# Optimization experiments

Measured on AMD Instinct MI355X. Metric: run time of the kernel, lower is better.

Reference implementation:

```python
import jax, jax.numpy as jnp
import numpy as np
import math

B, C, H, W = 2, 64, 64, 64
DI = 2 * C          # d_inner
N = 16              # d_state
R = math.ceil(C / 16)  # dt_rank
K = 3               # d_conv
L = H * W

PARAM_KEYS = [
    'pe_x_w', 'pe_x_b', 'rms_x_w', 'conv_x_w', 'conv_x_b',
    'pe_info_w', 'pe_info_b', 'rms_info_w', 'conv_info_w', 'conv_info_b',
    'pe_mask_w', 'pe_mask_b', 'rms_mask_w', 'conv_mask_w', 'conv_mask_b',
    'in_x_w', 'in_info_w', 'in_mask_w',
    'delta_w', 'dt_w', 'dt_b', 'B_w', 'C_w', 'A_log', 'out_w',
]


def setup_inputs():
    key = jax.random.key(0)
    ki = iter(jax.random.split(key, 40))
    def nrm(shape, scale=1.0):
        return jax.random.normal(next(ki), shape, jnp.float32) * scale
    sc, sdi, sr, sk = 1/np.sqrt(C), 1/np.sqrt(DI), 1/np.sqrt(R), 1/np.sqrt(K)
    inp = {}
    for name in ('up', 'mask', 'x', 'y', 'z'):
        inp[name] = nrm((B, C, H, W))
    for role in ('x', 'info', 'mask'):
        inp[f'pe_{role}_w'] = nrm((3, C, C), sc)
        inp[f'pe_{role}_b'] = jnp.zeros((3, C), jnp.float32)
        inp[f'rms_{role}_w'] = jnp.ones((3, C), jnp.float32)
        inp[f'conv_{role}_w'] = nrm((3, DI, K), sk)
        inp[f'conv_{role}_b'] = nrm((3, DI), sk)
    inp['in_x_w'] = nrm((3, 2 * DI, C), sc)
    inp['in_info_w'] = nrm((3, DI, C), sc)
    inp['in_mask_w'] = nrm((3, DI, C), sc)
    inp['delta_w'] = nrm((3, R, DI), sdi)
    inp['dt_w'] = nrm((3, DI, R), sr)
    rng = np.random.default_rng(0)
    dt = np.exp(rng.uniform(size=(3, DI)) * (np.log(0.1) - np.log(0.001)) + np.log(0.001)).clip(min=1e-4)
    inp['dt_b'] = jnp.asarray(np.log(-np.expm1(-dt)), jnp.float32)
    inp['B_w'] = nrm((3, N, DI), sdi)
    inp['C_w'] = nrm((3, N, DI), sdi)
    inp['A_log'] = jnp.tile(jnp.log(jnp.arange(1, N + 1, dtype=jnp.float32)), (3, DI, 1))
    inp['out_w'] = nrm((3, C, DI), sdi)
    return inp


def embed1x1(t, w, b):
    # PatchEmbed with patch_size=1: 1x1 conv then flatten to [B, L, C]
    y = jnp.einsum('bchw,oc->bohw', t, w) + b[None, :, None, None]
    bb, cc, hh, ww = y.shape
    return y.reshape(bb, cc, hh * ww).transpose(0, 2, 1)


def rms_norm(x, w, eps=1e-5):
    return x * jax.lax.rsqrt(jnp.mean(x * x, axis=-1, keepdims=True) + eps) * w


def causal_dwconv_silu(x, w, b):
    # x [B, D, L]; depthwise causal conv1d (left-pad K-1), then SiLU
    kk = w.shape[1]
    xp = jnp.pad(x, ((0, 0), (0, 0), (kk - 1, 0)))
    y = jax.lax.conv_general_dilated(
        xp, w[:, None, :], window_strides=(1,), padding='VALID',
        dimension_numbers=('NCH', 'OIH', 'NCH'), feature_group_count=w.shape[0])
    return jax.nn.silu(y + b[None, :, None])


def selective_scan(u, delta, A, Bm, Cm):
    # u, delta: [B, D, L]; A: [D, N]; Bm, Cm: [B, N, L]
    dA = jnp.exp(jnp.einsum('bdl,dn->lbdn', delta, A))           # [L,B,D,N]
    dBu = jnp.einsum('bdl,bnl,bdl->lbdn', delta, Bm, u)          # [L,B,D,N]
    Ct = Cm.transpose(2, 0, 1)                                   # [L,B,N]
    h0 = jnp.zeros((u.shape[0], u.shape[1], A.shape[1]), u.dtype)
    def step(h, inp):
        dA_t, dBu_t, C_t = inp
        h = dA_t * h + dBu_t
        return h, jnp.einsum('bdn,bn->bd', h, C_t)
    _, ys = jax.lax.scan(step, h0, (dA, dBu, Ct))
    return ys.transpose(1, 2, 0)                                 # [B,D,L]


def branch(xin, maskin, upin, p):
    bb, cc, hh, ww = xin.shape
    xe = rms_norm(embed1x1(xin, p['pe_x_w'], p['pe_x_b']), p['rms_x_w'])        # [B,L,C]
    xz = jnp.einsum('blc,dc->bdl', xe, p['in_x_w'])                              # [B,2DI,L]
    di = xz.shape[1] // 2
    xc, x_act = xz[:, :di], xz[:, di:]
    info = rms_norm(embed1x1(upin, p['pe_info_w'], p['pe_info_b']), p['rms_info_w'])
    info = jnp.einsum('blc,dc->bdl', info, p['in_info_w'])
    mk = rms_norm(embed1x1(maskin, p['pe_mask_w'], p['pe_mask_b']), p['rms_mask_w'])
    mk = jnp.einsum('blc,dc->bdl', mk, p['in_mask_w'])
    xc = causal_dwconv_silu(xc, p['conv_x_w'], p['conv_x_b'])
    mk = causal_dwconv_silu(mk, p['conv_mask_w'], p['conv_mask_b'])
    info = causal_dwconv_silu(info, p['conv_info_w'], p['conv_info_b'])
    # S6: delta from mask, B from info, C from x
    delta = jnp.einsum('bdl,rd->brl', mk, p['delta_w'])
    delta = jnp.einsum('brl,dr->bdl', delta, p['dt_w'])
    delta = jax.nn.softplus(delta + p['dt_b'][None, :, None])
    A = -jnp.exp(p['A_log'])
    Bm = jnp.einsum('bdl,nd->bnl', info, p['B_w'])
    Cm = jnp.einsum('bdl,nd->bnl', xc, p['C_w'])
    y = selective_scan(xc, delta, A, Bm, Cm)
    y = y * jax.nn.silu(x_act)
    y = jnp.einsum('bdl,cd->blc', y, p['out_w'])
    return y.transpose(0, 2, 1).reshape(bb, cc, hh, ww) + xin


def forward(up, mask, x, y, z, *params):
    pall = dict(zip(PARAM_KEYS, params))
    out = None
    for i, feat in enumerate((x, y, z)):
        p = {k: v[i] for k, v in pall.items()}
        o = branch(feat, mask, up, p)
        out = o if out is None else out + o
    return out


def reference(up, mask, x, y, z,
              pe_x_w, pe_x_b, rms_x_w, conv_x_w, conv_x_b,
              pe_info_w, pe_info_b, rms_info_w, conv_info_w, conv_info_b,
              pe_mask_w, pe_mask_b, rms_mask_w, conv_mask_w, conv_mask_b,
              in_x_w, in_info_w, in_mask_w,
              delta_w, dt_w, dt_b, B_w, C_w, A_log, out_w):
    return forward(up, mask, x, y, z,
                   pe_x_w, pe_x_b, rms_x_w, conv_x_w, conv_x_b,
                   pe_info_w, pe_info_b, rms_info_w, conv_info_w, conv_info_b,
                   pe_mask_w, pe_mask_b, rms_mask_w, conv_mask_w, conv_mask_b,
                   in_x_w, in_info_w, in_mask_w,
                   delta_w, dt_w, dt_b, B_w, C_w, A_log, out_w)
```

## Files before the change

kernel.cpp:

```cpp
#include <hip/hip_runtime.h>
#include <math.h>

namespace {

constexpr int NB = 3;
constexpr int BB = 2;
constexpr int CC = 64;
constexpr int LLEN = 4096;
constexpr int DI = 128;
constexpr int NN = 16;
constexpr int RR = 4;
constexpr int GG = 256;
constexpr int LC = 16;
constexpr int NSEQ = NB * BB * DI * NN;
constexpr size_t SBUF = (size_t)NB * BB * DI * LLEN;

typedef __attribute__((ext_vector_type(4))) float f32x4;
typedef __attribute__((ext_vector_type(8))) short bf16x8;

__device__ __forceinline__ float siluf(float v) { return v / (1.f + __expf(-v)); }

__device__ __forceinline__ short cvt_bf16(float f) {
    union { float f; unsigned u; } v; v.f = f;
    unsigned r = v.u + 0x7fffu + ((v.u >> 16) & 1u);
    return (short)(r >> 16);
}
__device__ __forceinline__ unsigned pack_bf16(float lo, float hi) {
    return ((unsigned)(unsigned short)cvt_bf16(hi) << 16) | (unsigned short)cvt_bf16(lo);
}
__device__ __forceinline__ bf16x8 pack8(float4 a, float4 b) {
    bf16x8 r;
    r[0] = cvt_bf16(a.x); r[1] = cvt_bf16(a.y); r[2] = cvt_bf16(a.z); r[3] = cvt_bf16(a.w);
    r[4] = cvt_bf16(b.x); r[5] = cvt_bf16(b.y); r[6] = cvt_bf16(b.z); r[7] = cvt_bf16(b.w);
    return r;
}

__global__ __launch_bounds__(256) void k1_embed(
    const float* __restrict__ up, const float* __restrict__ mask_,
    const float* __restrict__ fx, const float* __restrict__ fy, const float* __restrict__ fz,
    const float* __restrict__ pe_x_w, const float* __restrict__ pe_x_b, const float* __restrict__ rms_x_w,
    const float* __restrict__ pe_i_w, const float* __restrict__ pe_i_b, const float* __restrict__ rms_i_w,
    const float* __restrict__ pe_m_w, const float* __restrict__ pe_m_b, const float* __restrict__ rms_m_w,
    const float* __restrict__ in_x_w, const float* __restrict__ in_i_w, const float* __restrict__ in_m_w,
    float* __restrict__ xc_pre, float* __restrict__ x_act,
    float* __restrict__ info_pre, float* __restrict__ mk_pre)
{
    __shared__ short sE[64 * 64];
    __shared__ float red[4][64];
    __shared__ float sscl[64];

    int lt = blockIdx.x, job = blockIdx.y, b = blockIdx.z;
    int i = job / 3, r = job % 3;
    const float *src, *pw, *pb, *rw, *iw;
    if (r == 0) {
        src = (i == 0 ? fx : (i == 1 ? fy : fz));
        pw = pe_x_w + i * 4096; pb = pe_x_b + i * 64; rw = rms_x_w + i * 64;
        iw = in_x_w + (size_t)i * 256 * 64;
    } else if (r == 1) {
        src = up;
        pw = pe_i_w + i * 4096; pb = pe_i_b + i * 64; rw = rms_i_w + i * 64;
        iw = in_i_w + (size_t)i * 128 * 64;
    } else {
        src = mask_;
        pw = pe_m_w + i * 4096; pb = pe_m_b + i * 64; rw = rms_m_w + i * 64;
        iw = in_m_w + (size_t)i * 128 * 64;
    }
    int t = threadIdx.x;
    int w = t >> 6, lane = t & 63, lo = lane & 15, hi = lane >> 4;
    int l0 = lt * 64;
    const float* Xg = src + (size_t)b * 64 * LLEN;

    f32x4 acc1[4];
    #pragma unroll
    for (int nt = 0; nt < 4; ++nt) acc1[nt] = (f32x4){0.f, 0.f, 0.f, 0.f};

    #pragma unroll
    for (int ks = 0; ks < 2; ++ks) {
        const float* ap = pw + (16 * w + lo) * 64 + ks * 32 + hi * 8;
        bf16x8 a1 = pack8(*(const float4*)ap, *(const float4*)(ap + 4));
        #pragma unroll
        for (int nt = 0; nt < 4; ++nt) {
            const float* xc = Xg + (size_t)(ks * 32 + hi * 8) * LLEN + l0 + nt * 16 + lo;
            bf16x8 b1;
            #pragma unroll
            for (int j = 0; j < 8; ++j) b1[j] = cvt_bf16(xc[(size_t)j * LLEN]);
            acc1[nt] = __builtin_amdgcn_mfma_f32_16x16x32_bf16(a1, b1, acc1[nt], 0, 0, 0);
        }
    }

    float4 pbv = *(const float4*)&pb[16 * w + 4 * hi];
    float e_[4][4];
    #pragma unroll
    for (int nt = 0; nt < 4; ++nt) {
        e_[nt][0] = acc1[nt][0] + pbv.x;
        e_[nt][1] = acc1[nt][1] + pbv.y;
        e_[nt][2] = acc1[nt][2] + pbv.z;
        e_[nt][3] = acc1[nt][3] + pbv.w;
        float s = e_[nt][0] * e_[nt][0] + e_[nt][1] * e_[nt][1]
                + e_[nt][2] * e_[nt][2] + e_[nt][3] * e_[nt][3];
        s += __shfl_xor(s, 16);
        s += __shfl_xor(s, 32);
        if (lane < 16) red[w][nt * 16 + lo] = s;
    }
    __syncthreads();
    if (t < 64) {
        float s = red[0][t] + red[1][t] + red[2][t] + red[3][t];
        sscl[t] = rsqrtf(s * (1.f / 64.f) + 1e-5f);
    }
    __syncthreads();

    {
        int ob = 2 * w + (hi >> 1);
        #pragma unroll
        for (int nt = 0; nt < 4; ++nt) {
            float sc = sscl[16 * nt + lo];
            unsigned p0 = pack_bf16(e_[nt][0] * sc, e_[nt][1] * sc);
            unsigned p1 = pack_bf16(e_[nt][2] * sc, e_[nt][3] * sc);
            unsigned* p = (unsigned*)&sE[(16 * nt + lo) * 64 + (ob ^ (lo & 7)) * 8 + 4 * (hi & 1)];
            p[0] = p0; p[1] = p1;
        }
    }
    __syncthreads();

    bf16x8 b2[4][2];
    #pragma unroll
    for (int nt = 0; nt < 4; ++nt)
        #pragma unroll
        for (int ks = 0; ks < 2; ++ks) {
            int db = ks * 4 + hi;
            b2[nt][ks] = *(const bf16x8*)&sE[(16 * nt + lo) * 64 + (db ^ (lo & 7)) * 8];
        }

    size_t obase = ((size_t)(i * 2 + b)) * DI * LLEN;
    int MT = (r == 0) ? 4 : 2;
    for (int mm = 0; mm < MT; ++mm) {
        int m = MT * w + mm;
        bf16x8 a2[2];
        #pragma unroll
        for (int ks = 0; ks < 2; ++ks) {
            const float* wp = iw + (size_t)(16 * m + lo) * 64 + ks * 32 + hi * 8;
            float4 w0 = *(const float4*)wp;
            float4 w1 = *(const float4*)(wp + 4);
            float4 r0 = *(const float4*)&rw[ks * 32 + hi * 8];
            float4 r1 = *(const float4*)&rw[ks * 32 + hi * 8 + 4];
            w0.x *= r0.x; w0.y *= r0.y; w0.z *= r0.z; w0.w *= r0.w;
            w1.x *= r1.x; w1.y *= r1.y; w1.z *= r1.z; w1.w *= r1.w;
            a2[ks] = pack8(w0, w1);
        }
        f32x4 acc2[4];
        #pragma unroll
        for (int nt = 0; nt < 4; ++nt) acc2[nt] = (f32x4){0.f, 0.f, 0.f, 0.f};
        #pragma unroll
        for (int ks = 0; ks < 2; ++ks)
            #pragma unroll
            for (int nt = 0; nt < 4; ++nt)
                acc2[nt] = __builtin_amdgcn_mfma_f32_16x16x32_bf16(a2[ks], b2[nt][ks], acc2[nt], 0, 0, 0);

        int d0 = 16 * m + 4 * hi;
        float* dst; int dd = d0;
        if (r == 0) { if (d0 < 128) dst = xc_pre; else { dst = x_act; dd = d0 - 128; } }
        else if (r == 1) dst = info_pre;
        else dst = mk_pre;
        #pragma unroll
        for (int nt = 0; nt < 4; ++nt) {
            int l = l0 + 16 * nt + lo;
            *(float4*)&dst[obase + (size_t)l * DI + dd] =
                make_float4(acc2[nt][0], acc2[nt][1], acc2[nt][2], acc2[nt][3]);
        }
    }
}

__global__ __launch_bounds__(256) void k3_conv(
    const float* __restrict__ xc_pre, const float* __restrict__ info_pre, const float* __restrict__ mk_pre,
    const float* __restrict__ conv_x_w, const float* __restrict__ conv_x_b,
    const float* __restrict__ conv_i_w, const float* __restrict__ conv_i_b,
    const float* __restrict__ conv_m_w, const float* __restrict__ conv_m_b,
    const float* __restrict__ delta_w, const float* __restrict__ dt_w, const float* __restrict__ dt_b,
    const float* __restrict__ B_w, const float* __restrict__ C_w,
    float* __restrict__ u, float* __restrict__ delta,
    float* __restrict__ Bm, float* __restrict__ Cm)
{
    __shared__ __align__(16) float ot[64 * 128];
    __shared__ float rvec[4 * 64];

    int lt = blockIdx.x, ib = blockIdx.y, strm = blockIdx.z;
    int i = ib >> 1;
    int t = threadIdx.x;
    int l0 = lt * 64;
    size_t base = (size_t)ib * DI * LLEN;

    const float *inb, *cw, *cb;
    if (strm == 0)      { inb = mk_pre;   cw = conv_m_w + i * DI * 3; cb = conv_m_b + i * DI; }
    else if (strm == 1) { inb = info_pre; cw = conv_i_w + i * DI * 3; cb = conv_i_b + i * DI; }
    else                { inb = xc_pre;   cw = conv_x_w + i * DI * 3; cb = conv_x_b + i * DI; }

    {
        int d4 = t & 31, lq = t >> 5;
        int d = d4 * 4;
        float cw0[4], cw1[4], cw2[4], cbb[4];
        #pragma unroll
        for (int j = 0; j < 4; ++j) {
            cw0[j] = cw[(d + j) * 3 + 0];
            cw1[j] = cw[(d + j) * 3 + 1];
            cw2[j] = cw[(d + j) * 3 + 2];
            cbb[j] = cb[d + j];
        }
        int gl0 = l0 + lq * 8;
        float4 x0 = make_float4(0.f, 0.f, 0.f, 0.f), x1 = x0;
        if (gl0 >= 2) x0 = *(const float4*)&inb[base + (size_t)(gl0 - 2) * DI + d];
        if (gl0 >= 1) x1 = *(const float4*)&inb[base + (size_t)(gl0 - 1) * DI + d];
        #pragma unroll
        for (int li = 0; li < 8; ++li) {
            int l = lq * 8 + li;
            float4 x2 = *(const float4*)&inb[base + (size_t)(gl0 + li) * DI + d];
            float4 v;
            v.x = siluf(cw0[0] * x0.x + cw1[0] * x1.x + cw2[0] * x2.x + cbb[0]);
            v.y = siluf(cw0[1] * x0.y + cw1[1] * x1.y + cw2[1] * x2.y + cbb[1]);
            v.z = siluf(cw0[2] * x0.z + cw1[2] * x1.z + cw2[2] * x2.z + cbb[2]);
            v.w = siluf(cw0[3] * x0.w + cw1[3] * x1.w + cw2[3] * x2.w + cbb[3]);
            *(float4*)&ot[l * 128 + ((d4 * 4) ^ ((l & 7) << 2))] = v;
            if (strm == 2) *(float4*)&u[base + (size_t)(gl0 + li) * DI + d] = v;
            x0 = x1; x1 = x2;
        }
    }
    __syncthreads();

    if (strm == 0) {
        {
            int l = t & 63, r = t >> 6, sw = (l & 7) << 2;
            const float* dw = delta_w + i * RR * DI + r * DI;
            float acc = 0.f;
            #pragma unroll
            for (int d4 = 0; d4 < 32; ++d4) {
                float4 v = *(const float4*)&ot[l * 128 + ((d4 * 4) ^ sw)];
                int db = d4 * 4;
                acc += dw[db] * v.x + dw[db + 1] * v.y + dw[db + 2] * v.z + dw[db + 3] * v.w;
            }
            rvec[r * 64 + l] = acc;
        }
        __syncthreads();
        {
            int d = t & 127, lh = t >> 7;
            const float* dtw = dt_w + i * DI * RR + d * RR;
            float w0 = dtw[0], w1 = dtw[1], w2 = dtw[2], w3 = dtw[3];
            float bb = dt_b[i * DI + d];
            #pragma unroll 4
            for (int li = 0; li < 32; ++li) {
                int l = lh * 32 + li;
                float v = bb + w0 * rvec[l] + w1 * rvec[64 + l] + w2 * rvec[128 + l] + w3 * rvec[192 + l];
                float sp = (v > 20.f) ? v : log1pf(__expf(v));
                delta[base + (size_t)(l0 + l) * DI + d] = sp;
            }
        }
    } else {
        int l = t & 63, ng = t >> 6, sw = (l & 7) << 2;
        const float* wv = ((strm == 1) ? B_w : C_w) + i * NN * DI + ng * 4 * DI;
        float a0 = 0.f, a1 = 0.f, a2 = 0.f, a3 = 0.f;
        #pragma unroll
        for (int d4 = 0; d4 < 32; ++d4) {
            float4 v = *(const float4*)&ot[l * 128 + ((d4 * 4) ^ sw)];
            int db = d4 * 4;
            a0 += wv[db] * v.x + wv[db + 1] * v.y + wv[db + 2] * v.z + wv[db + 3] * v.w;
            a1 += wv[DI + db] * v.x + wv[DI + db + 1] * v.y + wv[DI + db + 2] * v.z + wv[DI + db + 3] * v.w;
            a2 += wv[2 * DI + db] * v.x + wv[2 * DI + db + 1] * v.y + wv[2 * DI + db + 2] * v.z + wv[2 * DI + db + 3] * v.w;
            a3 += wv[3 * DI + db] * v.x + wv[3 * DI + db + 1] * v.y + wv[3 * DI + db + 2] * v.z + wv[3 * DI + db + 3] * v.w;
        }
        float* dst = (strm == 1) ? Bm : Cm;
        *(float4*)&dst[((size_t)ib * LLEN + l0 + l) * NN + ng * 4] = make_float4(a0, a1, a2, a3);
    }
}

__global__ __launch_bounds__(128) void k4_scan1(
    const float* __restrict__ u, const float* __restrict__ delta,
    const float* __restrict__ Bm, const float* __restrict__ A_log,
    float* __restrict__ aprod, float* __restrict__ hend)
{
    __shared__ __align__(16) float sB[LC * 16];
    int g = blockIdx.x, ib = blockIdx.y, i = ib >> 1;
    int d = threadIdx.x;
    if (d < LC * 16 / 4)
        ((float4*)sB)[d] = ((const float4*)(Bm + ((size_t)ib * LLEN + (size_t)g * LC) * NN))[d];
    float A[16], h[16];
    {
        const float4* al = (const float4*)(A_log + ((size_t)i * DI + d) * NN);
        #pragma unroll
        for (int q = 0; q < 4; ++q) {
            float4 v = al[q];
            A[4 * q] = -__expf(v.x); A[4 * q + 1] = -__expf(v.y);
            A[4 * q + 2] = -__expf(v.z); A[4 * q + 3] = -__expf(v.w);
        }
    }
    #pragma unroll
    for (int n = 0; n < 16; ++n) h[n] = 0.f;
    float sdl = 0.f;
    __syncthreads();
    size_t base = ((size_t)ib * LLEN + (size_t)g * LC) * DI + d;
    #pragma unroll 4
    for (int li = 0; li < LC; ++li) {
        float dl = delta[base + li * DI];
        float du = dl * u[base + li * DI];
        sdl += dl;
        const float4* bl = (const float4*)(sB + li * 16);
        float4 b0 = bl[0], b1 = bl[1], b2 = bl[2], b3 = bl[3];
        h[0] = __expf(dl * A[0]) * h[0] + du * b0.x;  h[1] = __expf(dl * A[1]) * h[1] + du * b0.y;
        h[2] = __expf(dl * A[2]) * h[2] + du * b0.z;  h[3] = __expf(dl * A[3]) * h[3] + du * b0.w;
        h[4] = __expf(dl * A[4]) * h[4] + du * b1.x;  h[5] = __expf(dl * A[5]) * h[5] + du * b1.y;
        h[6] = __expf(dl * A[6]) * h[6] + du * b1.z;  h[7] = __expf(dl * A[7]) * h[7] + du * b1.w;
        h[8] = __expf(dl * A[8]) * h[8] + du * b2.x;  h[9] = __expf(dl * A[9]) * h[9] + du * b2.y;
        h[10] = __expf(dl * A[10]) * h[10] + du * b2.z; h[11] = __expf(dl * A[11]) * h[11] + du * b2.w;
        h[12] = __expf(dl * A[12]) * h[12] + du * b3.x; h[13] = __expf(dl * A[13]) * h[13] + du * b3.y;
        h[14] = __expf(dl * A[14]) * h[14] + du * b3.z; h[15] = __expf(dl * A[15]) * h[15] + du * b3.w;
    }
    size_t seq = ((size_t)ib * DI + d) * NN;
    float4* ap = (float4*)(aprod + (size_t)g * NSEQ + seq);
    float4* he = (float4*)(hend + (size_t)g * NSEQ + seq);
    #pragma unroll
    for (int q = 0; q < 4; ++q) {
        ap[q] = make_float4(__expf(A[4 * q] * sdl), __expf(A[4 * q + 1] * sdl),
                            __expf(A[4 * q + 2] * sdl), __expf(A[4 * q + 3] * sdl));
        he[q] = make_float4(h[4 * q], h[4 * q + 1], h[4 * q + 2], h[4 * q + 3]);
    }
}

__global__ __launch_bounds__(256) void k5_prefix(
    const float* __restrict__ aprod, const float* __restrict__ hend,
    float* __restrict__ hin)
{
    int s = blockIdx.x * 256 + threadIdx.x;
    float h = 0.f;
    #pragma unroll 8
    for (int g = 0; g < GG; ++g) {
        hin[(size_t)g * NSEQ + s] = h;
        h = aprod[(size_t)g * NSEQ + s] * h + hend[(size_t)g * NSEQ + s];
    }
}

__global__ __launch_bounds__(128) void k6_scan2(
    const float* __restrict__ u, const float* __restrict__ delta,
    const float* __restrict__ Bm, const float* __restrict__ Cm,
    const float* __restrict__ A_log, const float* __restrict__ hin,
    float* __restrict__ y)
{
    __shared__ __align__(16) float sB[LC * 16];
    __shared__ __align__(16) float sC[LC * 16];
    int g = blockIdx.x, ib = blockIdx.y, i = ib >> 1;
    int d = threadIdx.x;
    {
        const float4* bsrc = (const float4*)(Bm + ((size_t)ib * LLEN + (size_t)g * LC) * NN);
        const float4* csrc = (const float4*)(Cm + ((size_t)ib * LLEN + (size_t)g * LC) * NN);
        if (d < 64) ((float4*)sB)[d] = bsrc[d];
        else ((float4*)sC)[d - 64] = csrc[d - 64];
    }
    float A[16], h[16];
    {
        const float4* al = (const float4*)(A_log + ((size_t)i * DI + d) * NN);
        #pragma unroll
        for (int q = 0; q < 4; ++q) {
            float4 v = al[q];
            A[4 * q] = -__expf(v.x); A[4 * q + 1] = -__expf(v.y);
            A[4 * q + 2] = -__expf(v.z); A[4 * q + 3] = -__expf(v.w);
        }
    }
    {
        size_t seq = ((size_t)ib * DI + d) * NN;
        const float4* hp = (const float4*)(hin + (size_t)g * NSEQ + seq);
        #pragma unroll
        for (int q = 0; q < 4; ++q) {
            float4 v = hp[q];
            h[4 * q] = v.x; h[4 * q + 1] = v.y; h[4 * q + 2] = v.z; h[4 * q + 3] = v.w;
        }
    }
    __syncthreads();
    size_t base = ((size_t)ib * LLEN + (size_t)g * LC) * DI + d;
    #pragma unroll 4
    for (int li = 0; li < LC; ++li) {
        float dl = delta[base + li * DI];
        float du = dl * u[base + li * DI];
        const float4* bl = (const float4*)(sB + li * 16);
        const float4* cl = (const float4*)(sC + li * 16);
        float4 b0 = bl[0], b1 = bl[1], b2 = bl[2], b3 = bl[3];
        float4 c0 = cl[0], c1 = cl[1], c2 = cl[2], c3 = cl[3];
        float acc = 0.f;
        h[0] = __expf(dl * A[0]) * h[0] + du * b0.x;  acc += h[0] * c0.x;
        h[1] = __expf(dl * A[1]) * h[1] + du * b0.y;  acc += h[1] * c0.y;
        h[2] = __expf(dl * A[2]) * h[2] + du * b0.z;  acc += h[2] * c0.z;
        h[3] = __expf(dl * A[3]) * h[3] + du * b0.w;  acc += h[3] * c0.w;
        h[4] = __expf(dl * A[4]) * h[4] + du * b1.x;  acc += h[4] * c1.x;
        h[5] = __expf(dl * A[5]) * h[5] + du * b1.y;  acc += h[5] * c1.y;
        h[6] = __expf(dl * A[6]) * h[6] + du * b1.z;  acc += h[6] * c1.z;
        h[7] = __expf(dl * A[7]) * h[7] + du * b1.w;  acc += h[7] * c1.w;
        h[8] = __expf(dl * A[8]) * h[8] + du * b2.x;  acc += h[8] * c2.x;
        h[9] = __expf(dl * A[9]) * h[9] + du * b2.y;  acc += h[9] * c2.y;
        h[10] = __expf(dl * A[10]) * h[10] + du * b2.z; acc += h[10] * c2.z;
        h[11] = __expf(dl * A[11]) * h[11] + du * b2.w; acc += h[11] * c2.w;
        h[12] = __expf(dl * A[12]) * h[12] + du * b3.x; acc += h[12] * c3.x;
        h[13] = __expf(dl * A[13]) * h[13] + du * b3.y; acc += h[13] * c3.y;
        h[14] = __expf(dl * A[14]) * h[14] + du * b3.z; acc += h[14] * c3.z;
        h[15] = __expf(dl * A[15]) * h[15] + du * b3.w; acc += h[15] * c3.w;
        y[base + li * DI] = acc;
    }
}

__global__ __launch_bounds__(256) void k7_out(
    const float* __restrict__ y, const float* __restrict__ xact,
    const float* __restrict__ out_w,
    const float* __restrict__ fx, const float* __restrict__ fy, const float* __restrict__ fz,
    float* __restrict__ out)
{
    __shared__ short sG[64 * 128];
    int lt = blockIdx.x, b = blockIdx.y;
    int l0 = lt * 64;
    int t = threadIdx.x;
    int w = t >> 6, lane = t & 63, lo = lane & 15, hi = lane >> 4;

    f32x4 acc[4];
    #pragma unroll
    for (int nt = 0; nt < 4; ++nt) acc[nt] = (f32x4){0.f, 0.f, 0.f, 0.f};

    for (int i = 0; i < 3; ++i) {
        size_t base = ((size_t)(i * 2 + b)) * DI * LLEN;
        __syncthreads();
        #pragma unroll
        for (int p = 0; p < 8; ++p) {
            int idx = t + 256 * p;
            int d4 = idx & 31, l = idx >> 5;
            int d = d4 * 4;
            float4 yv = *(const float4*)&y[base + (size_t)(l0 + l) * DI + d];
            float4 xa = *(const float4*)&xact[base + (size_t)(l0 + l) * DI + d];
            float g0 = yv.x * siluf(xa.x), g1 = yv.y * siluf(xa.y);
            float g2 = yv.z * siluf(xa.z), g3 = yv.w * siluf(xa.w);
            int blk = d4 >> 1;
            int blks = (blk & 8) | ((blk ^ (l & 7)) & 7);
            unsigned* p32 = (unsigned*)&sG[l * 128 + blks * 8 + 4 * (d4 & 1)];
            p32[0] = pack_bf16(g0, g1);
            p32[1] = pack_bf16(g2, g3);
        }
        __syncthreads();

        const float* ow = out_w + (size_t)i * CC * DI;
        bf16x8 a[4];
        #pragma unroll
        for (int ks = 0; ks < 4; ++ks) {
            const float* ap = ow + (size_t)(16 * w + lo) * 128 + ks * 32 + hi * 8;
            a[ks] = pack8(*(const float4*)ap, *(const float4*)(ap + 4));
        }
        #pragma unroll
        for (int nt = 0; nt < 4; ++nt) {
            int l = 16 * nt + lo;
            #pragma unroll
            for (int ks = 0; ks < 4; ++ks) {
                int db = ks * 4 + hi;
                int blks = (db & 8) | ((db ^ (l & 7)) & 7);
                bf16x8 bv = *(const bf16x8*)&sG[l * 128 + blks * 8];
                acc[nt] = __builtin_amdgcn_mfma_f32_16x16x32_bf16(a[ks], bv, acc[nt], 0, 0, 0);
            }
        }
    }

    #pragma unroll
    for (int nt = 0; nt < 4; ++nt) {
        int l = l0 + 16 * nt + lo;
        int cbase = 16 * w + 4 * hi;
        #pragma unroll
        for (int rr = 0; rr < 4; ++rr) {
            int c = cbase + rr;
            size_t idx = ((size_t)b * CC + c) * LLEN + l;
            out[idx] = acc[nt][rr] + fx[idx] + fy[idx] + fz[idx];
        }
    }
}

}

extern "C" void kernel_launch(void* const* d_in, const int* in_sizes, int n_in,
                              void* d_out, int out_size, void* d_ws, size_t ws_size,
                              hipStream_t stream)
{
    (void)in_sizes; (void)n_in; (void)out_size; (void)ws_size;
    const float* up       = (const float*)d_in[0];
    const float* mask_    = (const float*)d_in[1];
    const float* fx       = (const float*)d_in[2];
    const float* fy       = (const float*)d_in[3];
    const float* fz       = (const float*)d_in[4];
    const float* pe_x_w   = (const float*)d_in[5];
    const float* pe_x_b   = (const float*)d_in[6];
    const float* rms_x_w  = (const float*)d_in[7];
    const float* conv_x_w = (const float*)d_in[8];
    const float* conv_x_b = (const float*)d_in[9];
    const float* pe_i_w   = (const float*)d_in[10];
    const float* pe_i_b   = (const float*)d_in[11];
    const float* rms_i_w  = (const float*)d_in[12];
    const float* conv_i_w = (const float*)d_in[13];
    const float* conv_i_b = (const float*)d_in[14];
    const float* pe_m_w   = (const float*)d_in[15];
    const float* pe_m_b   = (const float*)d_in[16];
    const float* rms_m_w  = (const float*)d_in[17];
    const float* conv_m_w = (const float*)d_in[18];
    const float* conv_m_b = (const float*)d_in[19];
    const float* in_x_w   = (const float*)d_in[20];
    const float* in_i_w   = (const float*)d_in[21];
    const float* in_m_w   = (const float*)d_in[22];
    const float* delta_w  = (const float*)d_in[23];
    const float* dt_w     = (const float*)d_in[24];
    const float* dt_b     = (const float*)d_in[25];
    const float* B_w      = (const float*)d_in[26];
    const float* C_w      = (const float*)d_in[27];
    const float* A_log    = (const float*)d_in[28];
    const float* out_w    = (const float*)d_in[29];
    float* out = (float*)d_out;

    float* ws = (float*)d_ws;
    const size_t S = SBUF;
    float* xc_pre   = ws;
    float* x_act    = ws + S;
    float* info_pre = ws + 2 * S;
    float* mk_pre   = ws + 3 * S;
    float* ubuf     = ws + 4 * S;
    float* dbuf     = ws + 5 * S;
    float* BmB      = ws + 6 * S;
    float* CmB      = BmB + (size_t)NB * BB * NN * LLEN;
    float* aprod = info_pre;
    float* hendb = mk_pre;
    float* hinb  = xc_pre;
    float* ybuf  = info_pre;

    hipLaunchKernelGGL(k1_embed, dim3(64, 9, 2), dim3(256), 0, stream,
        up, mask_, fx, fy, fz,
        pe_x_w, pe_x_b, rms_x_w, pe_i_w, pe_i_b, rms_i_w, pe_m_w, pe_m_b, rms_m_w,
        in_x_w, in_i_w, in_m_w, xc_pre, x_act, info_pre, mk_pre);

    hipLaunchKernelGGL(k3_conv, dim3(64, 6, 3), dim3(256), 0, stream,
        xc_pre, info_pre, mk_pre,
        conv_x_w, conv_x_b, conv_i_w, conv_i_b, conv_m_w, conv_m_b,
        delta_w, dt_w, dt_b, B_w, C_w, ubuf, dbuf, BmB, CmB);

    hipLaunchKernelGGL(k4_scan1, dim3(GG, 6), dim3(128), 0, stream,
        ubuf, dbuf, BmB, A_log, aprod, hendb);

    hipLaunchKernelGGL(k5_prefix, dim3(NSEQ / 256), dim3(256), 0, stream,
        aprod, hendb, hinb);

    hipLaunchKernelGGL(k6_scan2, dim3(GG, 6), dim3(128), 0, stream,
        ubuf, dbuf, BmB, CmB, A_log, hinb, ybuf);

    hipLaunchKernelGGL(k7_out, dim3(64, 2), dim3(256), 0, stream,
        ybuf, x_act, out_w, fx, fy, fz, out);
}
```

Measured before the change: 134.6 us.

## Store all intermediate workspace buffers in fp16 instead of fp32

Every intermediate buffer passed between kernels changes from fp32 to fp16: the projected activations, u, delta, B/C, the chunk products and end states, the carried-in states and y. Math inside each kernel stays fp32, with conversion on load and store. This halves global memory traffic across the memory-bound pipeline of embed, conv, two-pass scan and output. The cost is precision: fp16 range and rounding on delta, state products and hidden states can add error across the chunked scan.

```diff
diff --git a/kernel.cpp b/kernel.cpp
--- a/kernel.cpp
+++ b/kernel.cpp
@@ -15,8 +15,11 @@
 constexpr int NSEQ = NB * BB * DI * NN;
 constexpr size_t SBUF = (size_t)NB * BB * DI * LLEN;
 
+typedef _Float16 f16;
 typedef __attribute__((ext_vector_type(4))) float f32x4;
 typedef __attribute__((ext_vector_type(8))) short bf16x8;
+typedef __attribute__((ext_vector_type(4))) _Float16 f16x4;
+typedef __attribute__((ext_vector_type(8))) _Float16 f16x8;
 
 __device__ __forceinline__ float siluf(float v) { return v / (1.f + __expf(-v)); }
 
@@ -33,6 +36,12 @@
     r[0] = cvt_bf16(a.x); r[1] = cvt_bf16(a.y); r[2] = cvt_bf16(a.z); r[3] = cvt_bf16(a.w);
     r[4] = cvt_bf16(b.x); r[5] = cvt_bf16(b.y); r[6] = cvt_bf16(b.z); r[7] = cvt_bf16(b.w);
     return r;
+}
+__device__ __forceinline__ f16x4 to_h4(float a, float b, float c, float d) {
+    f16x4 r; r[0] = (f16)a; r[1] = (f16)b; r[2] = (f16)c; r[3] = (f16)d; return r;
+}
+__device__ __forceinline__ float4 to_f4(f16x4 v) {
+    return make_float4((float)v[0], (float)v[1], (float)v[2], (float)v[3]);
 }
 
 __global__ __launch_bounds__(256) void k1_embed(
@@ -42,8 +51,8 @@
     const float* __restrict__ pe_i_w, const float* __restrict__ pe_i_b, const float* __restrict__ rms_i_w,
     const float* __restrict__ pe_m_w, const float* __restrict__ pe_m_b, const float* __restrict__ rms_m_w,
     const float* __restrict__ in_x_w, const float* __restrict__ in_i_w, const float* __restrict__ in_m_w,
-    float* __restrict__ xc_pre, float* __restrict__ x_act,
-    float* __restrict__ info_pre, float* __restrict__ mk_pre)
+    f16* __restrict__ xc_pre, f16* __restrict__ x_act,
+    f16* __restrict__ info_pre, f16* __restrict__ mk_pre)
 {
     __shared__ short sE[64 * 64];
     __shared__ float red[4][64];
@@ -157,28 +166,28 @@
                 acc2[nt] = __builtin_amdgcn_mfma_f32_16x16x32_bf16(a2[ks], b2[nt][ks], acc2[nt], 0, 0, 0);
 
         int d0 = 16 * m + 4 * hi;
-        float* dst; int dd = d0;
+        f16* dst; int dd = d0;
         if (r == 0) { if (d0 < 128) dst = xc_pre; else { dst = x_act; dd = d0 - 128; } }
         else if (r == 1) dst = info_pre;
         else dst = mk_pre;
         #pragma unroll
         for (int nt = 0; nt < 4; ++nt) {
             int l = l0 + 16 * nt + lo;
-            *(float4*)&dst[obase + (size_t)l * DI + dd] =
-                make_float4(acc2[nt][0], acc2[nt][1], acc2[nt][2], acc2[nt][3]);
+            *(f16x4*)&dst[obase + (size_t)l * DI + dd] =
+                to_h4(acc2[nt][0], acc2[nt][1], acc2[nt][2], acc2[nt][3]);
         }
     }
 }
 
 __global__ __launch_bounds__(256) void k3_conv(
-    const float* __restrict__ xc_pre, const float* __restrict__ info_pre, const float* __restrict__ mk_pre,
+    const f16* __restrict__ xc_pre, const f16* __restrict__ info_pre, const f16* __restrict__ mk_pre,
     const float* __restrict__ conv_x_w, const float* __restrict__ conv_x_b,
     const float* __restrict__ conv_i_w, const float* __restrict__ conv_i_b,
     const float* __restrict__ conv_m_w, const float* __restrict__ conv_m_b,
     const float* __restrict__ delta_w, const float* __restrict__ dt_w, const float* __restrict__ dt_b,
     const float* __restrict__ B_w, const float* __restrict__ C_w,
-    float* __restrict__ u, float* __restrict__ delta,
-    float* __restrict__ Bm, float* __restrict__ Cm)
+    f16* __restrict__ u, f16* __restrict__ delta,
+    f16* __restrict__ Bm, f16* __restrict__ Cm)
 {
     __shared__ __align__(16) float ot[64 * 128];
     __shared__ float rvec[4 * 64];
@@ -189,7 +198,7 @@
     int l0 = lt * 64;
     size_t base = (size_t)ib * DI * LLEN;
 
-    const float *inb, *cw, *cb;
+    const f16 *inb; const float *cw, *cb;
     if (strm == 0)      { inb = mk_pre;   cw = conv_m_w + i * DI * 3; cb = conv_m_b + i * DI; }
     else if (strm == 1) { inb = info_pre; cw = conv_i_w + i * DI * 3; cb = conv_i_b + i * DI; }
     else                { inb = xc_pre;   cw = conv_x_w + i * DI * 3; cb = conv_x_b + i * DI; }
@@ -207,19 +216,19 @@
         }
         int gl0 = l0 + lq * 8;
         float4 x0 = make_float4(0.f, 0.f, 0.f, 0.f), x1 = x0;
-        if (gl0 >= 2) x0 = *(const float4*)&inb[base + (size_t)(gl0 - 2) * DI + d];
-        if (gl0 >= 1) x1 = *(const float4*)&inb[base + (size_t)(gl0 - 1) * DI + d];
+        if (gl0 >= 2) x0 = to_f4(*(const f16x4*)&inb[base + (size_t)(gl0 - 2) * DI + d]);
+        if (gl0 >= 1) x1 = to_f4(*(const f16x4*)&inb[base + (size_t)(gl0 - 1) * DI + d]);
         #pragma unroll
         for (int li = 0; li < 8; ++li) {
             int l = lq * 8 + li;
-            float4 x2 = *(const float4*)&inb[base + (size_t)(gl0 + li) * DI + d];
+            float4 x2 = to_f4(*(const f16x4*)&inb[base + (size_t)(gl0 + li) * DI + d]);
             float4 v;
             v.x = siluf(cw0[0] * x0.x + cw1[0] * x1.x + cw2[0] * x2.x + cbb[0]);
             v.y = siluf(cw0[1] * x0.y + cw1[1] * x1.y + cw2[1] * x2.y + cbb[1]);
             v.z = siluf(cw0[2] * x0.z + cw1[2] * x1.z + cw2[2] * x2.z + cbb[2]);
             v.w = siluf(cw0[3] * x0.w + cw1[3] * x1.w + cw2[3] * x2.w + cbb[3]);
             *(float4*)&ot[l * 128 + ((d4 * 4) ^ ((l & 7) << 2))] = v;
-            if (strm == 2) *(float4*)&u[base + (size_t)(gl0 + li) * DI + d] = v;
+            if (strm == 2) *(f16x4*)&u[base + (size_t)(gl0 + li) * DI + d] = to_h4(v.x, v.y, v.z, v.w);
             x0 = x1; x1 = x2;
         }
     }
@@ -249,7 +258,7 @@
                 int l = lh * 32 + li;
                 float v = bb + w0 * rvec[l] + w1 * rvec[64 + l] + w2 * rvec[128 + l] + w3 * rvec[192 + l];
                 float sp = (v > 20.f) ? v : log1pf(__expf(v));
-                delta[base + (size_t)(l0 + l) * DI + d] = sp;
+                delta[base + (size_t)(l0 + l) * DI + d] = (f16)sp;
             }
         }
     } else {
@@ -265,21 +274,23 @@
             a2 += wv[2 * DI + db] * v.x + wv[2 * DI + db + 1] * v.y + wv[2 * DI + db + 2] * v.z + wv[2 * DI + db + 3] * v.w;
             a3 += wv[3 * DI + db] * v.x + wv[3 * DI + db + 1] * v.y + wv[3 * DI + db + 2] * v.z + wv[3 * DI + db + 3] * v.w;
         }
-        float* dst = (strm == 1) ? Bm : Cm;
-        *(float4*)&dst[((size_t)ib * LLEN + l0 + l) * NN + ng * 4] = make_float4(a0, a1, a2, a3);
+        f16* dst = (strm == 1) ? Bm : Cm;
+        *(f16x4*)&dst[((size_t)ib * LLEN + l0 + l) * NN + ng * 4] = to_h4(a0, a1, a2, a3);
     }
 }
 
 __global__ __launch_bounds__(128) void k4_scan1(
-    const float* __restrict__ u, const float* __restrict__ delta,
-    const float* __restrict__ Bm, const float* __restrict__ A_log,
-    float* __restrict__ aprod, float* __restrict__ hend)
+    const f16* __restrict__ u, const f16* __restrict__ delta,
+    const f16* __restrict__ Bm, const float* __restrict__ A_log,
+    f16* __restrict__ aprod, f16* __restrict__ hend)
 {
     __shared__ __align__(16) float sB[LC * 16];
     int g = blockIdx.x, ib = blockIdx.y, i = ib >> 1;
     int d = threadIdx.x;
-    if (d < LC * 16 / 4)
-        ((float4*)sB)[d] = ((const float4*)(Bm + ((size_t)ib * LLEN + (size_t)g * LC) * NN))[d];
+    if (d < 64) {
+        f16x4 v = ((const f16x4*)(Bm + ((size_t)ib * LLEN + (size_t)g * LC) * NN))[d];
+        ((float4*)sB)[d] = to_f4(v);
+    }
     float A[16], h[16];
     {
         const float4* al = (const float4*)(A_log + ((size_t)i * DI + d) * NN);
@@ -297,8 +308,8 @@
     size_t base = ((size_t)ib * LLEN + (size_t)g * LC) * DI + d;
     #pragma unroll 4
     for (int li = 0; li < LC; ++li) {
-        float dl = delta[base + li * DI];
-        float du = dl * u[base + li * DI];
+        float dl = (float)delta[base + li * DI];
+        float du = dl * (float)u[base + li * DI];
         sdl += dl;
         const float4* bl = (const float4*)(sB + li * 16);
         float4 b0 = bl[0], b1 = bl[1], b2 = bl[2], b3 = bl[3];
@@ -312,44 +323,48 @@
         h[14] = __expf(dl * A[14]) * h[14] + du * b3.z; h[15] = __expf(dl * A[15]) * h[15] + du * b3.w;
     }
     size_t seq = ((size_t)ib * DI + d) * NN;
-    float4* ap = (float4*)(aprod + (size_t)g * NSEQ + seq);
-    float4* he = (float4*)(hend + (size_t)g * NSEQ + seq);
-    #pragma unroll
-    for (int q = 0; q < 4; ++q) {
-        ap[q] = make_float4(__expf(A[4 * q] * sdl), __expf(A[4 * q + 1] * sdl),
-                            __expf(A[4 * q + 2] * sdl), __expf(A[4 * q + 3] * sdl));
-        he[q] = make_float4(h[4 * q], h[4 * q + 1], h[4 * q + 2], h[4 * q + 3]);
+    f16x8* ap = (f16x8*)(aprod + (size_t)g * NSEQ + seq);
+    f16x8* he = (f16x8*)(hend + (size_t)g * NSEQ + seq);
+    #pragma unroll
+    for (int q = 0; q < 2; ++q) {
+        f16x8 av, hv;
+        #pragma unroll
+        for (int j = 0; j < 8; ++j) {
+            av[j] = (f16)__expf(A[8 * q + j] * sdl);
+            hv[j] = (f16)h[8 * q + j];
+        }
+        ap[q] = av; he[q] = hv;
     }
 }
 
 __global__ __launch_bounds__(256) void k5_prefix(
-    const float* __restrict__ aprod, const float* __restrict__ hend,
-    float* __restrict__ hin)
+    const f16* __restrict__ aprod, const f16* __restrict__ hend,
+    f16* __restrict__ hin)
 {
     int s = blockIdx.x * 256 + threadIdx.x;
     float h = 0.f;
     #pragma unroll 8
     for (int g = 0; g < GG; ++g) {
-        hin[(size_t)g * NSEQ + s] = h;
-        h = aprod[(size_t)g * NSEQ + s] * h + hend[(size_t)g * NSEQ + s];
+        hin[(size_t)g * NSEQ + s] = (f16)h;
+        h = (float)aprod[(size_t)g * NSEQ + s] * h + (float)hend[(size_t)g * NSEQ + s];
     }
 }
 
 __global__ __launch_bounds__(128) void k6_scan2(
-    const float* __restrict__ u, const float* __restrict__ delta,
-    const float* __restrict__ Bm, const float* __restrict__ Cm,
-    const float* __restrict__ A_log, const float* __restrict__ hin,
-    float* __restrict__ y)
+    const f16* __restrict__ u, const f16* __restrict__ delta,
+    const f16* __restrict__ Bm, const f16* __restrict__ Cm,
+    const float* __restrict__ A_log, const f16* __restrict__ hin,
+    f16* __restrict__ y)
 {
     __shared__ __align__(16) float sB[LC * 16];
     __shared__ __align__(16) float sC[LC * 16];
     int g = blockIdx.x, ib = blockIdx.y, i = ib >> 1;
     int d = threadIdx.x;
     {
-        const float4* bsrc = (const float4*)(Bm + ((size_t)ib * LLEN + (size_t)g * LC) * NN);
-        const float4* csrc = (const float4*)(Cm + ((size_t)ib * LLEN + (size_t)g * LC) * NN);
-        if (d < 64) ((float4*)sB)[d] = bsrc[d];
-        else ((float4*)sC)[d - 64] = csrc[d - 64];
+        const f16x4* bsrc = (const f16x4*)(Bm + ((size_t)ib * LLEN + (size_t)g * LC) * NN);
+        const f16x4* csrc = (const f16x4*)(Cm + ((size_t)ib * LLEN + (size_t)g * LC) * NN);
+        if (d < 64) ((float4*)sB)[d] = to_f4(bsrc[d]);
+        else ((float4*)sC)[d - 64] = to_f4(csrc[d - 64]);
     }
     float A[16], h[16];
     {
@@ -363,19 +378,20 @@
     }
     {
         size_t seq = ((size_t)ib * DI + d) * NN;
-        const float4* hp = (const float4*)(hin + (size_t)g * NSEQ + seq);
-        #pragma unroll
-        for (int q = 0; q < 4; ++q) {
-            float4 v = hp[q];
-            h[4 * q] = v.x; h[4 * q + 1] = v.y; h[4 * q + 2] = v.z; h[4 * q + 3] = v.w;
+        const f16x8* hp = (const f16x8*)(hin + (size_t)g * NSEQ + seq);
+        #pragma unroll
+        for (int q = 0; q < 2; ++q) {
+            f16x8 v = hp[q];
+            #pragma unroll
+            for (int j = 0; j < 8; ++j) h[8 * q + j] = (float)v[j];
         }
     }
     __syncthreads();
     size_t base = ((size_t)ib * LLEN + (size_t)g * LC) * DI + d;
     #pragma unroll 4
     for (int li = 0; li < LC; ++li) {
-        float dl = delta[base + li * DI];
-        float du = dl * u[base + li * DI];
+        float dl = (float)delta[base + li * DI];
+        float du = dl * (float)u[base + li * DI];
         const float4* bl = (const float4*)(sB + li * 16);
         const float4* cl = (const float4*)(sC + li * 16);
         float4 b0 = bl[0], b1 = bl[1], b2 = bl[2], b3 = bl[3];
@@ -397,12 +413,12 @@
         h[13] = __expf(dl * A[13]) * h[13] + du * b3.y; acc += h[13] * c3.y;
         h[14] = __expf(dl * A[14]) * h[14] + du * b3.z; acc += h[14] * c3.z;
         h[15] = __expf(dl * A[15]) * h[15] + du * b3.w; acc += h[15] * c3.w;
-        y[base + li * DI] = acc;
+        y[base + li * DI] = (f16)acc;
     }
 }
 
 __global__ __launch_bounds__(256) void k7_out(
-    const float* __restrict__ y, const float* __restrict__ xact,
+    const f16* __restrict__ y, const f16* __restrict__ xact,
     const float* __restrict__ out_w,
     const float* __restrict__ fx, const float* __restrict__ fy, const float* __restrict__ fz,
     float* __restrict__ out)
@@ -425,8 +441,8 @@
             int idx = t + 256 * p;
             int d4 = idx & 31, l = idx >> 5;
             int d = d4 * 4;
-            float4 yv = *(const float4*)&y[base + (size_t)(l0 + l) * DI + d];
-            float4 xa = *(const float4*)&xact[base + (size_t)(l0 + l) * DI + d];
+            float4 yv = to_f4(*(const f16x4*)&y[base + (size_t)(l0 + l) * DI + d]);
+            float4 xa = to_f4(*(const f16x4*)&xact[base + (size_t)(l0 + l) * DI + d]);
             float g0 = yv.x * siluf(xa.x), g1 = yv.y * siluf(xa.y);
             float g2 = yv.z * siluf(xa.z), g3 = yv.w * siluf(xa.w);
             int blk = d4 >> 1;
@@ -509,20 +525,20 @@
     const float* out_w    = (const float*)d_in[29];
     float* out = (float*)d_out;
 
-    float* ws = (float*)d_ws;
+    f16* ws = (f16*)d_ws;
     const size_t S = SBUF;
-    float* xc_pre   = ws;
-    float* x_act    = ws + S;
-    float* info_pre = ws + 2 * S;
-    float* mk_pre   = ws + 3 * S;
-    float* ubuf     = ws + 4 * S;
-    float* dbuf     = ws + 5 * S;
-    float* BmB      = ws + 6 * S;
-    float* CmB      = BmB + (size_t)NB * BB * NN * LLEN;
-    float* aprod = info_pre;
-    float* hendb = mk_pre;
-    float* hinb  = xc_pre;
-    float* ybuf  = info_pre;
+    f16* xc_pre   = ws;
+    f16* x_act    = ws + S;
+    f16* info_pre = ws + 2 * S;
+    f16* mk_pre   = ws + 3 * S;
+    f16* ubuf     = ws + 4 * S;
+    f16* dbuf     = ws + 5 * S;
+    f16* BmB      = ws + 6 * S;
+    f16* CmB      = BmB + (size_t)NB * BB * NN * LLEN;
+    f16* aprod = info_pre;
+    f16* hendb = mk_pre;
+    f16* hinb  = xc_pre;
+    f16* ybuf  = info_pre;
 
     hipLaunchKernelGGL(k1_embed, dim3(64, 9, 2), dim3(256), 0, stream,
         up, mask_, fx, fy, fz,
```

Result: no change. 133.0 us (-1.2%).
